# Kernel optimization log

Hardware: AMD Instinct MI355X
Metric: run time of the kernel (lower is better)

The kernel has to match this reference:

```python
import jax, jax.numpy as jnp
import numpy as np

B, S, F_IN, E = 512, 150, 75, 128
D, NH_M, DH_M, QKB = 256, 4, 64, 4
NB_M = D // QKB            # 64 block-diagonal blocks of size 4 for q/k/v proj
NH_S, DH_S = 4, 32
K = 4                      # causal conv kernel size
FF = 192                   # round_up(1.3*128, 64)


def _lin(k, fi, fo):
    return jax.random.normal(k, (fi, fo), jnp.float32) / np.sqrt(fi)


def setup_inputs():
    key = jax.random.key(0)
    ks = iter(jax.random.split(key, 64))
    p = {}
    p['x'] = jax.random.normal(next(ks), (B, S, F_IN), jnp.float32)
    p['w_in'] = _lin(next(ks), F_IN, E); p['b_in'] = jnp.zeros((E,), jnp.float32)
    p['ln0_w'] = jnp.ones((E,), jnp.float32)
    p['m_up_w'] = _lin(next(ks), E, 2 * D); p['m_up_b'] = jnp.zeros((2 * D,), jnp.float32)
    p['m_conv_w'] = jax.random.normal(next(ks), (D, K), jnp.float32) / np.sqrt(K)
    p['m_conv_b'] = jnp.zeros((D,), jnp.float32)
    for nm in ('q', 'k', 'v'):
        p['m_%s_w' % nm] = jax.random.normal(next(ks), (NB_M, QKB, QKB), jnp.float32) / np.sqrt(QKB)
        p['m_%s_b' % nm] = jnp.zeros((D,), jnp.float32)
    p['m_ig_w'] = _lin(next(ks), 3 * D, NH_M); p['m_ig_b'] = jnp.zeros((NH_M,), jnp.float32)
    p['m_fg_w'] = _lin(next(ks), 3 * D, NH_M); p['m_fg_b'] = jnp.full((NH_M,), 3.0, jnp.float32)
    p['m_norm_w'] = jnp.ones((D,), jnp.float32); p['m_skip'] = jnp.ones((D,), jnp.float32)
    p['m_down_w'] = _lin(next(ks), D, E); p['m_down_b'] = jnp.zeros((E,), jnp.float32)
    p['ln1_w'] = jnp.ones((E,), jnp.float32)
    p['s_conv_w'] = jax.random.normal(next(ks), (E, K), jnp.float32) / np.sqrt(K)
    p['s_conv_b'] = jnp.zeros((E,), jnp.float32)
    p['s_gate_w'] = jax.random.normal(next(ks), (4, NH_S, DH_S, DH_S), jnp.float32) / np.sqrt(DH_S)
    p['s_r'] = jax.random.normal(next(ks), (4, NH_S, DH_S, DH_S), jnp.float32) / np.sqrt(DH_S)
    fb = jnp.linspace(3.0, 6.0, NH_S * DH_S, dtype=jnp.float32).reshape(NH_S, DH_S)
    p['s_b'] = jnp.zeros((4, NH_S, DH_S), jnp.float32).at[1].set(fb)  # powerlaw-ish forget bias
    p['s_norm_w'] = jnp.ones((E,), jnp.float32)
    p['ln_ff_w'] = jnp.ones((E,), jnp.float32)
    p['ff_up_w'] = _lin(next(ks), E, 2 * FF); p['ff_up_b'] = jnp.zeros((2 * FF,), jnp.float32)
    p['ff_down_w'] = _lin(next(ks), FF, E); p['ff_down_b'] = jnp.zeros((E,), jnp.float32)
    p['post_w'] = jnp.ones((E,), jnp.float32)
    p['fc_w'] = _lin(next(ks), E, 1); p['fc_b'] = jnp.zeros((1,), jnp.float32)
    return p


def _layernorm(x, w, eps=1e-5):
    mu = jnp.mean(x, -1, keepdims=True)
    xc = x - mu
    var = jnp.mean(xc * xc, -1, keepdims=True)
    return xc * jax.lax.rsqrt(var + eps) * w


def _mhln(x, w, eps=1e-5):
    # x: (B,S,NH,DH), per-head group norm over DH; w: (NH,DH)
    mu = jnp.mean(x, -1, keepdims=True)
    xc = x - mu
    var = jnp.mean(xc * xc, -1, keepdims=True)
    return xc * jax.lax.rsqrt(var + eps) * w


def _causal_conv1d(x, w, b):
    # depthwise causal conv; x: (B,S,C), w: (C,K)
    C, Kk = w.shape
    xp = jnp.pad(x, ((0, 0), (Kk - 1, 0), (0, 0)))
    kern = jnp.transpose(w)[:, None, :]  # (K,1,C)
    y = jax.lax.conv_general_dilated(xp, kern, (1,), 'VALID',
        dimension_numbers=('NWC', 'WIO', 'NWC'), feature_group_count=C)
    return y + b


def _headwise(x, w, b=None):
    # block-diagonal (headwise) linear; w: (NB, out_pb, in_pb)
    nb = w.shape[0]
    xs = x.reshape(x.shape[:-1] + (nb, x.shape[-1] // nb))
    y = jnp.einsum('bsnd,nod->bsno', xs, w)
    y = y.reshape(x.shape[:-1] + (nb * w.shape[1],))
    return y if b is None else y + b


def _mlstm_parallel(q, k, v, ig, fg):
    # parallel stabilized mLSTM; q,k,v: (B,NH,S,DH); ig,fg: (B,NH,S)
    DH = q.shape[-1]
    Sl = q.shape[2]
    logf = jax.nn.log_sigmoid(fg)
    lfc = jnp.concatenate([jnp.zeros_like(logf[..., :1]), jnp.cumsum(logf, -1)], -1)
    fmat = lfc[..., :, None] - lfc[..., None, :]          # (B,NH,S+1,S+1)
    tril = jnp.tril(jnp.ones((Sl + 1, Sl + 1), bool))
    fmat = jnp.where(tril, fmat, -jnp.inf)[..., 1:, 1:]
    logD = fmat + ig[..., None, :]
    maxD = jnp.max(logD, -1, keepdims=True)
    Dm = jnp.exp(logD - maxD)
    qk = jnp.einsum('bhsd,bhtd->bhst', q, k) / np.sqrt(DH)
    C = qk * Dm
    norm = jnp.maximum(jnp.abs(jnp.sum(C, -1, keepdims=True)), jnp.exp(-maxD))
    return jnp.einsum('bhst,bhtd->bhsd', C / (norm + 1e-6), v)


def _forward(x, w_in, b_in, ln0_w, m_up_w, m_up_b, m_conv_w, m_conv_b,
             m_q_w, m_q_b, m_k_w, m_k_b, m_v_w, m_v_b, m_ig_w, m_ig_b,
             m_fg_w, m_fg_b, m_norm_w, m_skip, m_down_w, m_down_b, ln1_w,
             s_conv_w, s_conv_b, s_gate_w, s_r, s_b, s_norm_w, ln_ff_w,
             ff_up_w, ff_up_b, ff_down_w, ff_down_b, post_w, fc_w, fc_b):
    Bq = x.shape[0]
    h = x @ w_in + b_in                                   # input projection (dropout=eval identity)
    # ---- block 0: mLSTM (pre-LN residual) ----
    xn = _layernorm(h, ln0_w)
    up = xn @ m_up_w + m_up_b
    x_m, z = jnp.split(up, 2, -1)                         # (B,S,D) each
    xc = jax.nn.silu(_causal_conv1d(x_m, m_conv_w, m_conv_b))
    q = _headwise(xc, m_q_w, m_q_b)
    k = _headwise(xc, m_k_w, m_k_b)
    v = _headwise(x_m, m_v_w, m_v_b)
    if_in = jnp.concatenate([q, k, v], -1)                # (B,S,3D)
    ig = (if_in @ m_ig_w + m_ig_b).transpose(0, 2, 1)     # (B,NH,S)
    fg = (if_in @ m_fg_w + m_fg_b).transpose(0, 2, 1)
    toh = lambda t: t.reshape(Bq, S, NH_M, DH_M).transpose(0, 2, 1, 3)
    hcell = _mlstm_parallel(toh(q), toh(k), toh(v), ig, fg).transpose(0, 2, 1, 3)
    hn = _mhln(hcell, m_norm_w.reshape(NH_M, DH_M)).reshape(Bq, S, D)
    hs = (hn + m_skip * xc) * jax.nn.silu(z)              # learnable skip + output gate
    h = h + hs @ m_down_w + m_down_b
    # ---- block 1: sLSTM (vanilla recurrent) + gated FFN ----
    xn = _layernorm(h, ln1_w)
    xcs = jax.nn.silu(_causal_conv1d(xn, s_conv_w, s_conv_b))
    gi = _headwise(xcs, s_gate_w[0]); gf = _headwise(xcs, s_gate_w[1])
    gz = _headwise(xn, s_gate_w[2]); go = _headwise(xn, s_gate_w[3])
    tos = lambda t: t.reshape(Bq, S, NH_S, DH_S).transpose(1, 0, 2, 3)  # (S,B,NH,DH)
    gates = (tos(gi), tos(gf), tos(gz), tos(go))

    def step(carry, g):
        y, c, n, m = carry
        ry = jnp.einsum('bhd,ghdk->gbhk', y, s_r)
        ir = g[0] + ry[0] + s_b[0]
        fr = g[1] + ry[1] + s_b[1]
        zr = g[2] + ry[2] + s_b[2]
        orr = g[3] + ry[3] + s_b[3]
        logfplusm = m + jax.nn.log_sigmoid(fr)
        mnew = jnp.maximum(ir, logfplusm)
        igt = jnp.exp(ir - mnew)
        fgt = jnp.exp(logfplusm - mnew)
        cnew = fgt * c + igt * jnp.tanh(zr)
        nnew = fgt * n + igt
        ynew = jax.nn.sigmoid(orr) * cnew / nnew
        return (ynew, cnew, nnew, mnew), ynew

    z0 = jnp.zeros((Bq, NH_S, DH_S), x.dtype)
    m0 = jnp.full((Bq, NH_S, DH_S), -1e30, x.dtype)  # m0=-inf-ish => first step mnew=i, fgate=0
    _, ys = jax.lax.scan(step, (z0, z0, z0, m0), gates)
    ysl = _mhln(ys.transpose(1, 0, 2, 3), s_norm_w.reshape(NH_S, DH_S)).reshape(Bq, S, E)
    h = h + ysl
    xn = _layernorm(h, ln_ff_w)
    gpre, upj = jnp.split(xn @ ff_up_w + ff_up_b, 2, -1)
    h = h + (jax.nn.gelu(gpre, approximate=False) * upj) @ ff_down_w + ff_down_b
    # ---- post blocks norm + classifier head ----
    h = _layernorm(h, post_w)
    return h[:, -1, :] @ fc_w + fc_b


def reference(x, w_in, b_in, ln0_w, m_up_w, m_up_b, m_conv_w, m_conv_b,
              m_q_w, m_q_b, m_k_w, m_k_b, m_v_w, m_v_b, m_ig_w, m_ig_b,
              m_fg_w, m_fg_b, m_norm_w, m_skip, m_down_w, m_down_b, ln1_w,
              s_conv_w, s_conv_b, s_gate_w, s_r, s_b, s_norm_w, ln_ff_w,
              ff_up_w, ff_up_b, ff_down_w, ff_down_b, post_w, fc_w, fc_b):
    return _forward(x, w_in, b_in, ln0_w, m_up_w, m_up_b, m_conv_w, m_conv_b,
                    m_q_w, m_q_b, m_k_w, m_k_b, m_v_w, m_v_b, m_ig_w, m_ig_b,
                    m_fg_w, m_fg_b, m_norm_w, m_skip, m_down_w, m_down_b, ln1_w,
                    s_conv_w, s_conv_b, s_gate_w, s_r, s_b, s_norm_w, ln_ff_w,
                    ff_up_w, ff_up_b, ff_down_w, ff_down_b, post_w, fc_w, fc_b)
```

## Files before the change

kernel.cpp:

```cpp
#include <hip/hip_runtime.h>
#include <math.h>

#define B_ 512
#define S_ 150
#define FIN_ 75
#define E_ 128
#define D_ 256
#define FF_ 192
#define ROWS_ (B_*S_)

typedef _Float16 h4_t __attribute__((ext_vector_type(4)));
typedef _Float16 h8_t __attribute__((ext_vector_type(8)));
typedef float f4_t __attribute__((ext_vector_type(4)));

__device__ __forceinline__ float wsum(float v){
#pragma unroll
  for (int o=32;o;o>>=1) v += __shfl_xor(v,o,64);
  return v;
}
__device__ __forceinline__ float sigmoidf_(float x){ return 1.f/(1.f+expf(-x)); }
__device__ __forceinline__ float siluf_(float x){ return x/(1.f+expf(-x)); }
__device__ __forceinline__ float logsigf_(float x){ return fminf(x,0.f)-log1pf(expf(-fabsf(x))); }
__device__ __forceinline__ float dot4(float4 a, float4 b){ return a.x*b.x+a.y*b.y+a.z*b.z+a.w*b.w; }
__device__ __forceinline__ float hdot(float4 w, h4_t x){
  return w.x*(float)x[0] + w.y*(float)x[1] + w.z*(float)x[2] + w.w*(float)x[3];
}
__device__ __forceinline__ float4 h4f(h4_t v){
  return make_float4((float)v[0],(float)v[1],(float)v[2],(float)v[3]);
}
__device__ __forceinline__ float bsum128(float v, float* red2){
  v = wsum(v);
  __syncthreads();
  if ((threadIdx.x&63)==0) red2[threadIdx.x>>6]=v;
  __syncthreads();
  return red2[0]+red2[1];
}

__global__ __launch_bounds__(256) void k_inproj(const float* __restrict__ x, const float* __restrict__ w,
    const float* __restrict__ b, float* __restrict__ h){
  __shared__ float xl[16*FIN_];
  int row0 = blockIdx.x*16;
  int tid = threadIdx.x;
  for (int i=tid;i<16*FIN_;i+=256) xl[i] = x[(size_t)row0*FIN_ + i];
  __syncthreads();
  int o = tid & 127, rh = tid >> 7;
  float acc[8];
#pragma unroll
  for (int r=0;r<8;r++) acc[r]=0.f;
  for (int i=0;i<FIN_;i++){
    float wv = w[i*E_ + o];
#pragma unroll
    for (int r=0;r<8;r++) acc[r] += xl[(rh + 2*r)*FIN_ + i]*wv;
  }
  float bv = b[o];
#pragma unroll
  for (int r=0;r<8;r++) h[(size_t)(row0 + rh + 2*r)*E_ + o] = acc[r] + bv;
}

__global__ __launch_bounds__(256) void k_ln_up(const float* __restrict__ h, const float* __restrict__ lnw,
     const float* __restrict__ w, const float* __restrict__ bb,
     _Float16* __restrict__ xm, _Float16* __restrict__ z){
  __shared__ float xl[8*E_];
  int row0 = blockIdx.x*8; int tid = threadIdx.x;
  for (int i=tid;i<8*E_;i+=256) xl[i] = h[(size_t)row0*E_ + i];
  __syncthreads();
  int wave = tid>>6, lane = tid&63;
  for (int rr = wave; rr < 8; rr += 4){
    float x0 = xl[rr*E_+lane], x1 = xl[rr*E_+lane+64];
    float mu = wsum(x0+x1) * (1.f/E_);
    float d0=x0-mu, d1=x1-mu;
    float var = wsum(d0*d0+d1*d1)*(1.f/E_);
    float rs = rsqrtf(var+1e-5f);
    xl[rr*E_+lane] = d0*rs*lnw[lane];
    xl[rr*E_+lane+64] = d1*rs*lnw[lane+64];
  }
  __syncthreads();
  float a0[8], a1[8];
#pragma unroll
  for (int r=0;r<8;r++){a0[r]=0.f;a1[r]=0.f;}
  int o = tid;
  for (int i=0;i<E_;i+=4){
    float w0v[4], w1v[4];
#pragma unroll
    for (int ii=0;ii<4;ii++){ w0v[ii] = w[(i+ii)*512+o]; w1v[ii]=w[(i+ii)*512+o+256]; }
#pragma unroll
    for (int r=0;r<8;r++){
      float4 xr = *(const float4*)&xl[r*E_+i];
      a0[r] += xr.x*w0v[0] + xr.y*w0v[1] + xr.z*w0v[2] + xr.w*w0v[3];
      a1[r] += xr.x*w1v[0] + xr.y*w1v[1] + xr.z*w1v[2] + xr.w*w1v[3];
    }
  }
  float b0 = bb[o], b1 = bb[o+256];
#pragma unroll
  for (int r=0;r<8;r++){
    xm[(size_t)(row0+r)*D_ + o] = (_Float16)(a0[r]+b0);
    z [(size_t)(row0+r)*D_ + o] = (_Float16)(a1[r]+b1);
  }
}

__global__ __launch_bounds__(256) void k_conv_qkv(const _Float16* __restrict__ xm,
    const float* __restrict__ cw, const float* __restrict__ cb,
    const float* __restrict__ qw, const float* __restrict__ qb2,
    const float* __restrict__ kw, const float* __restrict__ kb2,
    const float* __restrict__ vw, const float* __restrict__ vb2,
    const float* __restrict__ igw, const float* __restrict__ igb,
    const float* __restrict__ fgw, const float* __restrict__ fgb,
    _Float16* __restrict__ xc, float* __restrict__ ig, float* __restrict__ fg){
  __shared__ float xml[4][D_];
  __shared__ float xcl[D_];
  __shared__ float part[4][8];
  int row = blockIdx.x; int b = row/S_; int s = row - b*S_;
  int c = threadIdx.x;
#pragma unroll
  for (int j=0;j<4;j++){
    int sj = s-3+j;
    xml[j][c] = (sj>=0)? (float)xm[(size_t)(row-3+j)*D_ + c] : 0.f;
  }
  __syncthreads();
  float4 wc = *(const float4*)&cw[c*4];
  float cv = cb[c] + wc.x*xml[0][c] + wc.y*xml[1][c] + wc.z*xml[2][c] + wc.w*xml[3][c];
  cv = siluf_(cv);
  xcl[c] = cv;
  xc[(size_t)row*D_ + c] = (_Float16)cv;
  int nb = c>>2, rr = c&3;
  float4 vw4 = *(const float4*)&vw[nb*16 + rr*4];
  float4 xv4 = *(const float4*)&xml[3][nb*4];
  float vv = vb2[c] + dot4(vw4, xv4);
  __syncthreads();
  float4 qw4 = *(const float4*)&qw[nb*16 + rr*4];
  float4 kw4 = *(const float4*)&kw[nb*16 + rr*4];
  float4 xc4 = *(const float4*)&xcl[nb*4];
  float qv = qb2[c] + dot4(qw4, xc4);
  float kv = kb2[c] + dot4(kw4, xc4);
  float4 wiq = *(const float4*)&igw[c*4];
  float4 wik = *(const float4*)&igw[(256+c)*4];
  float4 wiv = *(const float4*)&igw[(512+c)*4];
  float4 wfq = *(const float4*)&fgw[c*4];
  float4 wfk = *(const float4*)&fgw[(256+c)*4];
  float4 wfv = *(const float4*)&fgw[(512+c)*4];
  float p[8];
  p[0] = qv*wiq.x + kv*wik.x + vv*wiv.x;
  p[1] = qv*wiq.y + kv*wik.y + vv*wiv.y;
  p[2] = qv*wiq.z + kv*wik.z + vv*wiv.z;
  p[3] = qv*wiq.w + kv*wik.w + vv*wiv.w;
  p[4] = qv*wfq.x + kv*wfk.x + vv*wfv.x;
  p[5] = qv*wfq.y + kv*wfk.y + vv*wfv.y;
  p[6] = qv*wfq.z + kv*wfk.z + vv*wfv.z;
  p[7] = qv*wfq.w + kv*wfk.w + vv*wfv.w;
#pragma unroll
  for (int j=0;j<8;j++) p[j] = wsum(p[j]);
  int wave = c>>6, lane = c&63;
  if (lane==0){
#pragma unroll
    for (int j=0;j<8;j++) part[wave][j]=p[j];
  }
  __syncthreads();
  if (c < 8){
    float t4 = part[0][c]+part[1][c]+part[2][c]+part[3][c];
    int g = c&3;
    if (c<4) ig[(size_t)(b*4+g)*S_ + s] = t4 + igb[g];
    else     fg[(size_t)(b*4+g)*S_ + s] = t4 + fgb[g];
  }
}

__global__ __launch_bounds__(256) void k_mlstm(_Float16* xcio,
    const _Float16* __restrict__ xm, const _Float16* __restrict__ z,
    const float* __restrict__ qw, const float* __restrict__ qb2,
    const float* __restrict__ kw, const float* __restrict__ kb2,
    const float* __restrict__ vw, const float* __restrict__ vb2,
    const float* __restrict__ ig, const float* __restrict__ fg,
    const float* __restrict__ nw, const float* __restrict__ skip){
  __shared__ __align__(16) _Float16 kt[160*72];
  __shared__ __align__(16) _Float16 vT[64*184];
  __shared__ __align__(16) _Float16 ct[4][16*40];
  __shared__ float lfc[S_+1];
  __shared__ float igl[S_];
  __shared__ float mxl[S_];
  int bh = blockIdx.x; int b = bh>>2; int hh = bh&3;
  int tid = threadIdx.x; int wave = tid>>6, lane = tid&63;
  int quad = lane>>4, lm = lane&15;
  _Float16* xcg = xcio + (size_t)b*S_*D_ + hh*64;
  const _Float16* xmg = xm + (size_t)b*S_*D_ + hh*64;
  const _Float16* zg  = z  + (size_t)b*S_*D_ + hh*64;
  for (int i=tid;i<160*64;i+=256){
    int t=i>>6, d=i&63;
    float kvv=0.f, vvv=0.f;
    if (t<S_){
      int nb=d>>2, dd=d&3;
      h4_t xk = *(const h4_t*)&xcg[(size_t)t*D_+(nb<<2)];
      h4_t xv = *(const h4_t*)&xmg[(size_t)t*D_+(nb<<2)];
      float4 wk = *(const float4*)&kw[((hh*16+nb)<<4)+(dd<<2)];
      float4 wv = *(const float4*)&vw[((hh*16+nb)<<4)+(dd<<2)];
      kvv = kb2[hh*64+d]+hdot(wk,xk);
      vvv = vb2[hh*64+d]+hdot(wv,xv);
    }
    kt[t*72+d]=(_Float16)kvv;
    vT[d*184+t]=(_Float16)vvv;
  }
  if (tid<S_){ igl[tid]=ig[(size_t)bh*S_+tid]; mxl[tid]=logsigf_(fg[(size_t)bh*S_+tid]); }
  __syncthreads();
  if (tid==0){
    float run=0.f, rm=-3.0e38f;
    lfc[0]=0.f;
    for (int t=0;t<S_;t++){
      run += mxl[t];
      lfc[t+1]=run;
      float gv = igl[t]-run;
      rm = fmaxf(rm,gv);
      mxl[t] = run + rm;
    }
  }
  __syncthreads();
  float nwv[4], skv[4];
#pragma unroll
  for (int dt=0;dt<4;dt++){ nwv[dt]=nw[hh*64+dt*16+lm]; skv[dt]=skip[hh*64+dt*16+lm]; }
  _Float16* ctw = ct[wave];
  for (int qi=wave; qi<10; qi+=4){
    int s0=qi*16;
    int srow=s0+quad*4;
    int sq = s0+lm; if (sq>S_-1) sq=S_-1;
    const _Float16* xrow = &xcg[(size_t)sq*D_];
    h8_t qf0, qf1;
#pragma unroll
    for (int f=0; f<2; f++){
      int d0 = f*32 + quad*8;
      h4_t xa = *(const h4_t*)&xrow[d0];
      h4_t xb = *(const h4_t*)&xrow[d0+4];
      float4 xaf=h4f(xa), xbf=h4f(xb);
      int nb0 = (hh*16 + (d0>>2))<<4;
#pragma unroll
      for (int j=0;j<4;j++){
        float4 wr = *(const float4*)&qw[nb0 + j*4];
        float qv = qb2[hh*64+d0+j] + dot4(wr, xaf);
        if (f==0) qf0[j]=(_Float16)qv; else qf1[j]=(_Float16)qv;
      }
#pragma unroll
      for (int j=0;j<4;j++){
        float4 wr = *(const float4*)&qw[nb0 + 16 + j*4];
        float qv = qb2[hh*64+d0+4+j] + dot4(wr, xbf);
        if (f==0) qf0[4+j]=(_Float16)qv; else qf1[4+j]=(_Float16)qv;
      }
    }
    f4_t acc0={0,0,0,0},acc1={0,0,0,0},acc2={0,0,0,0},acc3={0,0,0,0};
    float rsum[4]={0.f,0.f,0.f,0.f};
    float lfs[4], mxs[4]; bool sv[4];
#pragma unroll
    for (int r=0;r<4;r++){
      int s=srow+r; sv[r]=(s<S_);
      int sc = sv[r]? s : S_-1;
      lfs[r]=lfc[sc+1]; mxs[r]=mxl[sc];
    }
    int npair=(qi+2)>>1;
    for (int tp=0; tp<npair; tp++){
#pragma unroll
      for (int half=0; half<2; half++){
        int ti=2*tp+half;
        f4_t aq={0,0,0,0};
        if (ti<=qi){
          int t0=ti*16;
          h8_t kb0=*(const h8_t*)&kt[(t0+lm)*72+quad*8];
          h8_t kb1=*(const h8_t*)&kt[(t0+lm)*72+32+quad*8];
          aq=__builtin_amdgcn_mfma_f32_16x16x32_f16(qf0,kb0,aq,0,0,0);
          aq=__builtin_amdgcn_mfma_f32_16x16x32_f16(qf1,kb1,aq,0,0,0);
        }
        int t=ti*16+lm;
        bool tv = (t<S_);
        float lfT = tv? lfc[t+1]:0.f;
        float igT = tv? igl[t]:0.f;
#pragma unroll
        for (int r=0;r<4;r++){
          float coef=0.f;
          if (tv && sv[r] && t<=srow+r){
            coef = aq[r]*0.125f*__expf(lfs[r]-lfT+igT-mxs[r]);
          }
          rsum[r]+=coef;
          ctw[(quad*4+r)*40 + half*16 + lm] = (_Float16)coef;
        }
      }
      asm volatile("s_waitcnt lgkmcnt(0)" ::: "memory");
      h8_t af=*(const h8_t*)&ctw[lm*40+quad*8];
      int tb=tp*32+quad*8;
      h8_t bv0=*(const h8_t*)&vT[(0*16+lm)*184+tb];
      h8_t bv1=*(const h8_t*)&vT[(1*16+lm)*184+tb];
      h8_t bv2=*(const h8_t*)&vT[(2*16+lm)*184+tb];
      h8_t bv3=*(const h8_t*)&vT[(3*16+lm)*184+tb];
      acc0=__builtin_amdgcn_mfma_f32_16x16x32_f16(af,bv0,acc0,0,0,0);
      acc1=__builtin_amdgcn_mfma_f32_16x16x32_f16(af,bv1,acc1,0,0,0);
      acc2=__builtin_amdgcn_mfma_f32_16x16x32_f16(af,bv2,acc2,0,0,0);
      acc3=__builtin_amdgcn_mfma_f32_16x16x32_f16(af,bv3,acc3,0,0,0);
    }
#pragma unroll
    for (int r=0;r<4;r++){
      float v_=rsum[r];
      v_+=__shfl_xor(v_,1,64); v_+=__shfl_xor(v_,2,64);
      v_+=__shfl_xor(v_,4,64); v_+=__shfl_xor(v_,8,64);
      rsum[r]=v_;
    }
    float nrm[4];
#pragma unroll
    for (int r=0;r<4;r++) nrm[r]=fmaxf(fabsf(rsum[r]), __expf(-mxs[r]))+1e-6f;
#pragma unroll
    for (int r=0;r<4;r++){
      if (!sv[r]) continue;
      int s=srow+r;
      float o0=acc0[r]/nrm[r], o1=acc1[r]/nrm[r], o2=acc2[r]/nrm[r], o3=acc3[r]/nrm[r];
      float ss=o0+o1+o2+o3;
      ss+=__shfl_xor(ss,1,64); ss+=__shfl_xor(ss,2,64); ss+=__shfl_xor(ss,4,64); ss+=__shfl_xor(ss,8,64);
      float mu=ss*(1.f/64.f);
      float d0=o0-mu,d1=o1-mu,d2=o2-mu,d3=o3-mu;
      float vv=d0*d0+d1*d1+d2*d2+d3*d3;
      vv+=__shfl_xor(vv,1,64); vv+=__shfl_xor(vv,2,64); vv+=__shfl_xor(vv,4,64); vv+=__shfl_xor(vv,8,64);
      float rs=rsqrtf(vv*(1.f/64.f)+1e-5f);
      size_t rowoff=(size_t)s*D_;
      float dd4[4]={d0,d1,d2,d3};
#pragma unroll
      for (int dt=0;dt<4;dt++){
        float hn = dd4[dt]*rs*nwv[dt];
        float xcv=(float)xcg[rowoff+dt*16+lm];
        float zv =(float)zg [rowoff+dt*16+lm];
        xcg[rowoff+dt*16+lm]=(_Float16)((hn+skv[dt]*xcv)*siluf_(zv));
      }
    }
  }
}

__global__ __launch_bounds__(256) void k_down(const _Float16* __restrict__ hs, const float* __restrict__ w,
    const float* __restrict__ bb, float* __restrict__ h){
  __shared__ float hl[8*D_];
  int row0 = blockIdx.x*8; int tid = threadIdx.x;
  for (int i=tid;i<8*D_;i+=256) hl[i] = (float)hs[(size_t)row0*D_ + i];
  __syncthreads();
  int o = tid&127, rh = tid>>7;
  float acc[4]={0.f,0.f,0.f,0.f};
  for (int i=0;i<D_;i+=4){
    float wv[4];
#pragma unroll
    for (int ii=0;ii<4;ii++) wv[ii] = w[(i+ii)*E_ + o];
#pragma unroll
    for (int r=0;r<4;r++){
      float4 xv = *(const float4*)&hl[(rh+2*r)*D_ + i];
      acc[r] += xv.x*wv[0]+xv.y*wv[1]+xv.z*wv[2]+xv.w*wv[3];
    }
  }
  float bv = bb[o];
#pragma unroll
  for (int r=0;r<4;r++){
    size_t idx = (size_t)(row0+rh+2*r)*E_ + o;
    h[idx] += acc[r] + bv;
  }
}

__global__ __launch_bounds__(256) void k_lnconv(const float* __restrict__ h, const float* __restrict__ lnw,
    const float* __restrict__ cw, const float* __restrict__ cb, _Float16* __restrict__ xcs){
  __shared__ float xn[19][E_];
  int b = blockIdx.x/10, chunk = blockIdx.x - b*10;
  int s0 = chunk*16;
  int tid=threadIdx.x, wave=tid>>6, lane=tid&63;
  for (int ii=wave; ii<19; ii+=4){
    int sg = s0-3+ii;
    if (sg>=0 && sg<S_){
      size_t off = (size_t)(b*S_+sg)*E_;
      float x0=h[off+lane], x1=h[off+lane+64];
      float mu=wsum(x0+x1)*(1.f/E_);
      float d0=x0-mu,d1=x1-mu;
      float var=wsum(d0*d0+d1*d1)*(1.f/E_);
      float rs=rsqrtf(var+1e-5f);
      xn[ii][lane]=d0*rs*lnw[lane];
      xn[ii][lane+64]=d1*rs*lnw[lane+64];
    } else { xn[ii][lane]=0.f; xn[ii][lane+64]=0.f; }
  }
  __syncthreads();
  int ch=tid&127, rh=tid>>7;
  float4 w4 = *(const float4*)&cw[ch*4];
  float bv = cb[ch];
  for (int r=rh; r<16; r+=2){
    int s=s0+r;
    if (s<S_){
      float acc = bv + w4.x*xn[r][ch] + w4.y*xn[r+1][ch] + w4.z*xn[r+2][ch] + w4.w*xn[r+3][ch];
      xcs[(size_t)(b*S_+s)*E_+ch] = (_Float16)siluf_(acc);
    }
  }
}

__global__ __launch_bounds__(128) void k_gates8(const _Float16* __restrict__ xcs, const float* __restrict__ h,
    const float* __restrict__ lnw, const float* __restrict__ gw,
    _Float16* __restrict__ gi, _Float16* __restrict__ gf,
    _Float16* __restrict__ gz, _Float16* __restrict__ go){
  __shared__ float xcl[E_], xnl[E_], red2[2];
  int row0 = blockIdx.x*8;
  int t = threadIdx.x;
  int hh = t>>5, o = t&31;
  const float* w0 = gw + (((0*4+hh)*32+o)<<5);
  const float* w1 = gw + (((1*4+hh)*32+o)<<5);
  const float* w2 = gw + (((2*4+hh)*32+o)<<5);
  const float* w3 = gw + (((3*4+hh)*32+o)<<5);
  float4 w0v[8], w1v[8], w2v[8], w3v[8];
#pragma unroll
  for (int d=0;d<8;d++){
    w0v[d]=*(const float4*)&w0[d*4]; w1v[d]=*(const float4*)&w1[d*4];
    w2v[d]=*(const float4*)&w2[d*4]; w3v[d]=*(const float4*)&w3[d*4];
  }
  float lnwv = lnw[t];
  for (int rr=0; rr<8; rr++){
    int row = row0+rr; int b = row/S_; int s = row - b*S_;
    float hv = h[(size_t)row*E_+t];
    float mu = bsum128(hv, red2)*(1.f/E_);
    float dd = hv-mu;
    float var = bsum128(dd*dd, red2)*(1.f/E_);
    xnl[t] = dd*rsqrtf(var+1e-5f)*lnwv;
    xcl[t] = (float)xcs[(size_t)row*E_+t];
    __syncthreads();
    float a0=0.f,a1=0.f,a2=0.f,a3=0.f;
    const float* xch = &xcl[hh*32]; const float* xnh = &xnl[hh*32];
#pragma unroll
    for (int d=0; d<8; d++){
      float4 xc4 = *(const float4*)&xch[d*4];
      float4 xn4 = *(const float4*)&xnh[d*4];
      a0 += dot4(w0v[d], xc4);
      a1 += dot4(w1v[d], xc4);
      a2 += dot4(w2v[d], xn4);
      a3 += dot4(w3v[d], xn4);
    }
    size_t oidx = ((size_t)s*B_ + b)*E_ + t;
    gi[oidx]=(_Float16)a0; gf[oidx]=(_Float16)a1; gz[oidx]=(_Float16)a2; go[oidx]=(_Float16)a3;
    __syncthreads();
  }
}

__global__ __launch_bounds__(128) void k_scan(const _Float16* __restrict__ gi, const _Float16* __restrict__ gf,
    const _Float16* __restrict__ gz, const _Float16* __restrict__ go,
    const float* __restrict__ sr, const float* __restrict__ sb, float* __restrict__ yl){
  __shared__ _Float16 srt[16384];
  int b = blockIdx.x; int t = threadIdx.x;
  for (int i=t;i<16384;i+=128){
    int g = i>>12; int rem = i&4095; int hh = rem>>10; int d = (rem>>5)&31; int kk = i&31;
    srt[(((hh*32+d)*32 + kk)<<2) + g] = (_Float16)sr[i];
  }
  __syncthreads();
  int hh = t>>5; int lane = t&63; int kk = t&31;
  float sb0 = sb[t], sb1 = sb[128+t], sb2 = sb[256+t], sb3 = sb[384+t];
  float y=0.f,cst=0.f,nst=0.f,mst=-1e30f;
  size_t base0 = (size_t)b*E_ + t;
  float gc0 = (float)gi[base0], gc1 = (float)gf[base0], gc2 = (float)gz[base0], gc3 = (float)go[base0];
  const _Float16* srh = srt + hh*4096;
  for (int s=0;s<S_;s++){
    int sn = (s+1 < S_)? s+1 : s;
    size_t nidx = ((size_t)sn*B_ + b)*E_ + t;
    float n0 = (float)gi[nidx], n1 = (float)gf[nidx], n2 = (float)gz[nidx], n3 = (float)go[nidx];
    float ry0=0.f,ry1=0.f,ry2=0.f,ry3=0.f;
#pragma unroll 8
    for (int d=0; d<32; d++){
      float yv = __shfl(y, (lane & 32) + d, 64);
      float4 w = h4f(*(const h4_t*)&srh[(d*32 + kk)<<2]);
      ry0 += yv*w.x; ry1 += yv*w.y; ry2 += yv*w.z; ry3 += yv*w.w;
    }
    float ir = gc0 + ry0 + sb0;
    float fr = gc1 + ry1 + sb1;
    float zr = gc2 + ry2 + sb2;
    float orr= gc3 + ry3 + sb3;
    float lfm = mst + logsigf_(fr);
    float mn = fmaxf(ir, lfm);
    float igt = expf(ir - mn);
    float fgt = expf(lfm - mn);
    cst = fgt*cst + igt*tanhf(zr);
    nst = fgt*nst + igt;
    mst = mn;
    y = sigmoidf_(orr)*cst/nst;
    gc0=n0; gc1=n1; gc2=n2; gc3=n3;
  }
  yl[(size_t)b*E_ + t] = y;
}

__global__ __launch_bounds__(128) void k_head(const float* __restrict__ h, const float* __restrict__ yl,
   const float* __restrict__ snw, const float* __restrict__ lnffw,
   const float* __restrict__ upw, const float* __restrict__ upb,
   const float* __restrict__ dww, const float* __restrict__ dwb,
   const float* __restrict__ postw, const float* __restrict__ fcw, const float* __restrict__ fcb,
   float* __restrict__ out){
  __shared__ float ylsh[E_], xnf[E_], up[2*FF_], gg[FF_], red2[2];
  int b = blockIdx.x; int t = threadIdx.x;
  float yv = yl[(size_t)b*E_+t];
  ylsh[t] = yv;
  __syncthreads();
  int base = (t>>5)<<5;
  float mu=0.f;
  for (int d=0;d<32;d++) mu += ylsh[base+d];
  mu *= (1.f/32.f);
  float var=0.f;
  for (int d=0;d<32;d++){ float dd = ylsh[base+d]-mu; var += dd*dd; }
  var *= (1.f/32.f);
  float hn = (yv-mu)*rsqrtf(var+1e-5f)*snw[t];
  float h1 = h[((size_t)b*S_ + (S_-1))*E_ + t] + hn;
  float mu1 = bsum128(h1, red2)*(1.f/E_);
  float d1 = h1-mu1;
  float var1 = bsum128(d1*d1, red2)*(1.f/E_);
  xnf[t] = d1*rsqrtf(var1+1e-5f)*lnffw[t];
  __syncthreads();
  float u0=upb[t], u1=upb[t+128], u2=upb[t+256];
  for (int i=0;i<E_;i++){
    float x = xnf[i];
    u0 += x*upw[i*384+t];
    u1 += x*upw[i*384+t+128];
    u2 += x*upw[i*384+t+256];
  }
  up[t]=u0; up[t+128]=u1; up[t+256]=u2;
  __syncthreads();
  for (int j=t;j<FF_;j+=128){
    float gp = up[j];
    gg[j] = 0.5f*gp*(1.f+erff(gp*0.70710678118f))*up[FF_+j];
  }
  __syncthreads();
  float acc = dwb[t];
  for (int j=0;j<FF_;j++) acc += gg[j]*dww[j*E_+t];
  float h2 = h1 + acc;
  float mu2 = bsum128(h2, red2)*(1.f/E_);
  float d2 = h2-mu2;
  float var2 = bsum128(d2*d2, red2)*(1.f/E_);
  float hp = d2*rsqrtf(var2+1e-5f)*postw[t];
  float pr = bsum128(hp*fcw[t], red2);
  if (t==0) out[b] = pr + fcb[0];
}

extern "C" void kernel_launch(void* const* d_in, const int* in_sizes, int n_in,
                              void* d_out, int out_size, void* d_ws, size_t ws_size,
                              hipStream_t stream){
  const float* x        = (const float*)d_in[0];
  const float* w_in     = (const float*)d_in[1];
  const float* b_in     = (const float*)d_in[2];
  const float* ln0_w    = (const float*)d_in[3];
  const float* m_up_w   = (const float*)d_in[4];
  const float* m_up_b   = (const float*)d_in[5];
  const float* m_conv_w = (const float*)d_in[6];
  const float* m_conv_b = (const float*)d_in[7];
  const float* m_q_w    = (const float*)d_in[8];
  const float* m_q_b    = (const float*)d_in[9];
  const float* m_k_w    = (const float*)d_in[10];
  const float* m_k_b    = (const float*)d_in[11];
  const float* m_v_w    = (const float*)d_in[12];
  const float* m_v_b    = (const float*)d_in[13];
  const float* m_ig_w   = (const float*)d_in[14];
  const float* m_ig_b   = (const float*)d_in[15];
  const float* m_fg_w   = (const float*)d_in[16];
  const float* m_fg_b   = (const float*)d_in[17];
  const float* m_norm_w = (const float*)d_in[18];
  const float* m_skip   = (const float*)d_in[19];
  const float* m_down_w = (const float*)d_in[20];
  const float* m_down_b = (const float*)d_in[21];
  const float* ln1_w    = (const float*)d_in[22];
  const float* s_conv_w = (const float*)d_in[23];
  const float* s_conv_b = (const float*)d_in[24];
  const float* s_gate_w = (const float*)d_in[25];
  const float* s_r      = (const float*)d_in[26];
  const float* s_b      = (const float*)d_in[27];
  const float* s_norm_w = (const float*)d_in[28];
  const float* ln_ff_w  = (const float*)d_in[29];
  const float* ff_up_w  = (const float*)d_in[30];
  const float* ff_up_b  = (const float*)d_in[31];
  const float* ff_down_w= (const float*)d_in[32];
  const float* ff_down_b= (const float*)d_in[33];
  const float* post_w   = (const float*)d_in[34];
  const float* fc_w     = (const float*)d_in[35];
  const float* fc_b     = (const float*)d_in[36];
  float* out = (float*)d_out;
  float* wsf = (float*)d_ws;

  float*     h  = wsf;
  _Float16*  A  = (_Float16*)(wsf + 9830400);
  _Float16*  Bz = (_Float16*)(wsf + 19660800);
  _Float16*  C  = (_Float16*)(wsf + 29491200);
  float*     ig = wsf + 39321600;
  float*     fg = wsf + 39628800;
  float*     yl = wsf + 39936000;

  k_inproj<<<ROWS_/16, 256, 0, stream>>>(x, w_in, b_in, h);
  k_ln_up<<<ROWS_/8, 256, 0, stream>>>(h, ln0_w, m_up_w, m_up_b, A, Bz);
  k_conv_qkv<<<ROWS_, 256, 0, stream>>>(A, m_conv_w, m_conv_b, m_q_w, m_q_b, m_k_w, m_k_b,
       m_v_w, m_v_b, m_ig_w, m_ig_b, m_fg_w, m_fg_b, C, ig, fg);
  k_mlstm<<<B_*4, 256, 0, stream>>>(C, A, Bz, m_q_w, m_q_b, m_k_w, m_k_b, m_v_w, m_v_b,
       ig, fg, m_norm_w, m_skip);
  k_down<<<ROWS_/8, 256, 0, stream>>>(C, m_down_w, m_down_b, h);
  _Float16* xcs = A;
  _Float16* gz  = A + 9830400;
  _Float16* gi  = Bz;
  _Float16* gf  = Bz + 9830400;
  _Float16* go  = C;
  k_lnconv<<<B_*10, 256, 0, stream>>>(h, ln1_w, s_conv_w, s_conv_b, xcs);
  k_gates8<<<ROWS_/8, 128, 0, stream>>>(xcs, h, ln1_w, s_gate_w, gi, gf, gz, go);
  k_scan<<<B_, 128, 0, stream>>>(gi, gf, gz, go, s_r, s_b, yl);
  k_head<<<B_, 128, 0, stream>>>(h, yl, s_norm_w, ln_ff_w, ff_up_w, ff_up_b,
       ff_down_w, ff_down_b, post_w, fc_w, fc_b, out);
}
```

Baseline: 1.371 ms.

## Split sLSTM scan per head with recurrent weights held in registers

The sequential scan now launches one 64-lane wavefront per (batch, head) instead of one 128-thread block per batch. Each half-wave computes two of the four gate recurrences, and the halves swap partial sums with a xor shuffle. The recurrent matrix moves from shared memory into 64 per-lane registers, which removes the LDS staging, the barrier and the per-step LDS reads. In exchange, both halves redo the state update, the register count goes up, and every block reloads its slice of the weights from global memory.

```diff
diff --git a/kernel.cpp b/kernel.cpp
--- a/kernel.cpp
+++ b/kernel.cpp
@@ -427,33 +427,42 @@
   }
 }
 
-__global__ __launch_bounds__(128) void k_scan(const _Float16* __restrict__ gi, const _Float16* __restrict__ gf,
+__global__ __launch_bounds__(64) void k_scan(const _Float16* __restrict__ gi, const _Float16* __restrict__ gf,
     const _Float16* __restrict__ gz, const _Float16* __restrict__ go,
     const float* __restrict__ sr, const float* __restrict__ sb, float* __restrict__ yl){
-  __shared__ _Float16 srt[16384];
-  int b = blockIdx.x; int t = threadIdx.x;
-  for (int i=t;i<16384;i+=128){
-    int g = i>>12; int rem = i&4095; int hh = rem>>10; int d = (rem>>5)&31; int kk = i&31;
-    srt[(((hh*32+d)*32 + kk)<<2) + g] = (_Float16)sr[i];
-  }
-  __syncthreads();
-  int hh = t>>5; int lane = t&63; int kk = t&31;
-  float sb0 = sb[t], sb1 = sb[128+t], sb2 = sb[256+t], sb3 = sb[384+t];
+  int bh = blockIdx.x; int b = bh>>2; int hh = bh&3;
+  int lane = threadIdx.x; int kk = lane&31; int half = lane>>5;
+  int gA = half*2, gB = half*2+1;
+  const float* srA = sr + (size_t)((gA*4+hh)*32)*32 + kk;
+  const float* srB = sr + (size_t)((gB*4+hh)*32)*32 + kk;
+  float wA[32], wB[32];
+#pragma unroll
+  for (int d=0; d<32; d++){
+    wA[d] = (float)(_Float16)srA[d*32];
+    wB[d] = (float)(_Float16)srB[d*32];
+  }
+  int c = hh*32 + kk;
+  float sb0 = sb[c], sb1 = sb[128+c], sb2 = sb[256+c], sb3 = sb[384+c];
   float y=0.f,cst=0.f,nst=0.f,mst=-1e30f;
-  size_t base0 = (size_t)b*E_ + t;
+  size_t base0 = (size_t)b*E_ + c;
   float gc0 = (float)gi[base0], gc1 = (float)gf[base0], gc2 = (float)gz[base0], gc3 = (float)go[base0];
-  const _Float16* srh = srt + hh*4096;
   for (int s=0;s<S_;s++){
     int sn = (s+1 < S_)? s+1 : s;
-    size_t nidx = ((size_t)sn*B_ + b)*E_ + t;
+    size_t nidx = ((size_t)sn*B_ + b)*E_ + c;
     float n0 = (float)gi[nidx], n1 = (float)gf[nidx], n2 = (float)gz[nidx], n3 = (float)go[nidx];
-    float ry0=0.f,ry1=0.f,ry2=0.f,ry3=0.f;
-#pragma unroll 8
+    float ryA=0.f, ryB=0.f;
+#pragma unroll
     for (int d=0; d<32; d++){
-      float yv = __shfl(y, (lane & 32) + d, 64);
-      float4 w = h4f(*(const h4_t*)&srh[(d*32 + kk)<<2]);
-      ry0 += yv*w.x; ry1 += yv*w.y; ry2 += yv*w.z; ry3 += yv*w.w;
-    }
+      float yv = __shfl(y, d, 64);
+      ryA += yv*wA[d];
+      ryB += yv*wB[d];
+    }
+    float oA = __shfl_xor(ryA, 32, 64);
+    float oB = __shfl_xor(ryB, 32, 64);
+    float ry0 = half? oA  : ryA;
+    float ry1 = half? oB  : ryB;
+    float ry2 = half? ryA : oA;
+    float ry3 = half? ryB : oB;
     float ir = gc0 + ry0 + sb0;
     float fr = gc1 + ry1 + sb1;
     float zr = gc2 + ry2 + sb2;
@@ -468,7 +477,7 @@
     y = sigmoidf_(orr)*cst/nst;
     gc0=n0; gc1=n1; gc2=n2; gc3=n3;
   }
-  yl[(size_t)b*E_ + t] = y;
+  if (half==0) yl[(size_t)b*E_ + c] = y;
 }
 
 __global__ __launch_bounds__(128) void k_head(const float* __restrict__ h, const float* __restrict__ yl,
@@ -586,7 +595,7 @@
   _Float16* go  = C;
   k_lnconv<<<B_*10, 256, 0, stream>>>(h, ln1_w, s_conv_w, s_conv_b, xcs);
   k_gates8<<<ROWS_/8, 128, 0, stream>>>(xcs, h, ln1_w, s_gate_w, gi, gf, gz, go);
-  k_scan<<<B_, 128, 0, stream>>>(gi, gf, gz, go, s_r, s_b, yl);
+  k_scan<<<B_*4, 64, 0, stream>>>(gi, gf, gz, go, s_r, s_b, yl);
   k_head<<<B_, 128, 0, stream>>>(h, yl, s_norm_w, ln_ff_w, ff_up_w, ff_up_b,
        ff_down_w, ff_down_b, post_w, fc_w, fc_b, out);
 }
```

After: 1.332 ms. 2.8% less time.
